# Kernel tuning notes

Measured on AMD Instinct MI355X. Metric: run time of the kernel, lower is better.

The kernel has to match this reference:

```python
import jax, jax.numpy as jnp
import numpy as np

N = 8192
IN_F = 512
OUT_F = 64
ALPHA = 0.2  # LeakyReLU negative slope
NEG_INF = -9e15


def setup_inputs() -> dict:
    key = jax.random.key(0)
    k1, k2, k3, k4 = jax.random.split(key, 4)
    # xavier_uniform-style scale (gain=1.414)
    w_bound = 1.414 * np.sqrt(6.0 / (IN_F + OUT_F))
    a_bound = 1.414 * np.sqrt(6.0 / (2 * OUT_F + 1))
    return {
        "input": jax.random.normal(k1, (N, IN_F), dtype=jnp.float32),
        "adj": jax.random.randint(k2, (N, N), 0, 2, dtype=jnp.int32),
        "W": jax.random.uniform(k3, (IN_F, OUT_F), jnp.float32, -w_bound, w_bound),
        "a": jax.random.uniform(k4, (2 * OUT_F, 1), jnp.float32, -a_bound, a_bound),
        "sig_sample_size": 512,
    }


def reference(input, adj, W, a, sig_sample_size):
    h = input @ W  # [N, F]
    # Split 'a' so e_ij = leakyrelu(a1.h_i + a2.h_j) without the N*N*2F repeat/cat
    a1, a2 = a[:OUT_F, 0], a[OUT_F:, 0]  # [F], [F]
    e = jax.nn.leaky_relu((h @ a1)[:, None] + (h @ a2)[None, :], negative_slope=ALPHA)  # [N, N]
    attention = jnp.where(adj > 0, e, NEG_INF)
    attention = jax.nn.softmax(attention, axis=1)
    sig_scores = jnp.sum(attention, axis=0)  # [N]
    _, indices = jax.lax.top_k(sig_scores, sig_sample_size)
    return indices
```

## Files before the change

kernel.cpp:

```cpp
#include <hip/hip_runtime.h>
#include <stdint.h>

#define NROW 8192
#define IN_F 512
#define OUT_F 64
#define ALPHA 0.2f

__device__ float  g_wa1[IN_F];
__device__ float  g_wa2[IN_F];
__device__ float  g_f1[NROW];
__device__ float  g_f2[NROW];
__device__ float  g_E2f[NROW];
__device__ float  g_F2f[NROW];
__device__ double g_E2d[NROW];
__device__ double g_F2d[NROW];
__device__ double g_accp[NROW];
__device__ double g_accn[NROW];
__device__ double g_G1[NROW];
__device__ double g_H1[NROW];
__device__ double g_colsum[NROW];
__device__ unsigned long long g_mask[(size_t)NROW * 128];

__global__ void prep_wa(const float* __restrict__ W, const float* __restrict__ a) {
    int k = threadIdx.x;
    if (k < IN_F) {
        double s1 = 0.0, s2 = 0.0;
        for (int t = 0; t < OUT_F; ++t) {
            double w = (double)W[k * OUT_F + t];
            s1 += w * (double)a[t];
            s2 += w * (double)a[OUT_F + t];
        }
        g_wa1[k] = (float)s1;
        g_wa2[k] = (float)s2;
        #pragma unroll
        for (int i = 0; i < 16; ++i) g_colsum[k * 16 + i] = 0.0;
    }
}

__global__ void __launch_bounds__(256) compute_f(const float* __restrict__ in) {
    int wave = threadIdx.x >> 6, lane = threadIdx.x & 63;
    int row = blockIdx.x * 4 + wave;
    const float4* in4  = (const float4*)(in + (size_t)row * IN_F);
    const float4* wa14 = (const float4*)g_wa1;
    const float4* wa24 = (const float4*)g_wa2;
    double s1 = 0.0, s2 = 0.0;
    #pragma unroll
    for (int half = 0; half < 2; ++half) {
        int idx = half * 64 + lane;
        float4 x = in4[idx];
        float4 u = wa14[idx];
        float4 v = wa24[idx];
        s1 += (double)x.x*u.x + (double)x.y*u.y + (double)x.z*u.z + (double)x.w*u.w;
        s2 += (double)x.x*v.x + (double)x.y*v.y + (double)x.z*v.z + (double)x.w*v.w;
    }
    #pragma unroll
    for (int off = 32; off > 0; off >>= 1) {
        s1 += __shfl_down(s1, off, 64);
        s2 += __shfl_down(s2, off, 64);
    }
    if (lane == 0) {
        float f1 = (float)s1, f2 = (float)s2;
        g_f1[row] = f1; g_f2[row] = f2;
        double e2 = exp((double)f2), g2 = exp(0.2 * (double)f2);
        g_E2d[row] = e2;        g_F2d[row] = g2;
        g_E2f[row] = (float)e2; g_F2f[row] = (float)g2;
    }
}

__global__ void __launch_bounds__(256) row_z_mask(const int* __restrict__ adj) {
    __shared__ float E2s[NROW];
    __shared__ float F2s[NROW];
    __shared__ double zp[16], zn[16];
    int tid = threadIdx.x;
    int wave = tid >> 6, lane = tid & 63;
    for (int k = tid; k < NROW / 4; k += 256) {
        ((float4*)E2s)[k] = ((const float4*)g_E2f)[k];
        ((float4*)F2s)[k] = ((const float4*)g_F2f)[k];
    }
    __syncthreads();
    int row0 = blockIdx.x * 4;
    for (int r = 0; r < 4; ++r) {
        int row = row0 + r;
        float f1r = g_f1[row];
        float Ft = expf(-0.2f * f1r);
        const int4* arow = (const int4*)(adj + (size_t)row * NROW) + wave * 512;
        unsigned long long myword = 0;
        double accp = 0.0, accn = 0.0;
        #pragma unroll
        for (int it = 0; it < 8; ++it) {
            int4 av = arow[it * 64 + lane];
            int colbase = wave * 2048 + it * 256 + lane * 4;
            float4 E2v = *(const float4*)&E2s[colbase];
            float4 F2v = *(const float4*)&F2s[colbase];
            bool p0 = av.x > 0, p1 = av.y > 0, p2 = av.z > 0, p3 = av.w > 0;
            unsigned long long b0 = __ballot(p0), b1 = __ballot(p1);
            unsigned long long b2 = __ballot(p2), b3 = __ballot(p3);
            int bl = it * 4;
            if (lane == bl)     myword = b0;
            if (lane == bl + 1) myword = b1;
            if (lane == bl + 2) myword = b2;
            if (lane == bl + 3) myword = b3;
            bool q0 = F2v.x > Ft, q1 = F2v.y > Ft, q2 = F2v.z > Ft, q3 = F2v.w > Ft;
            accp += (p0 && q0) ? (double)E2v.x : 0.0;
            accn += (p0 && !q0) ? (double)F2v.x : 0.0;
            accp += (p1 && q1) ? (double)E2v.y : 0.0;
            accn += (p1 && !q1) ? (double)F2v.y : 0.0;
            accp += (p2 && q2) ? (double)E2v.z : 0.0;
            accn += (p2 && !q2) ? (double)F2v.z : 0.0;
            accp += (p3 && q3) ? (double)E2v.w : 0.0;
            accn += (p3 && !q3) ? (double)F2v.w : 0.0;
        }
        if (lane < 32) g_mask[(size_t)row * 128 + wave * 32 + lane] = myword;
        #pragma unroll
        for (int off = 32; off > 0; off >>= 1) {
            accp += __shfl_down(accp, off, 64);
            accn += __shfl_down(accn, off, 64);
        }
        if (lane == 0) { zp[r * 4 + wave] = accp; zn[r * 4 + wave] = accn; }
    }
    __syncthreads();
    if (tid < 4) {
        g_accp[row0 + tid] = zp[tid*4+0] + zp[tid*4+1] + zp[tid*4+2] + zp[tid*4+3];
        g_accn[row0 + tid] = zn[tid*4+0] + zn[tid*4+1] + zn[tid*4+2] + zn[tid*4+3];
    }
}

__global__ void __launch_bounds__(256) prep_gh() {
    int i = blockIdx.x * 256 + threadIdx.x;
    double f1d = (double)g_f1[i];
    double e1 = exp(f1d), h1 = exp(0.2 * f1d);
    double Z = e1 * g_accp[i] + h1 * g_accn[i];
    double zinv = 1.0 / Z;
    g_G1[i] = e1 * zinv;
    g_H1[i] = h1 * zinv;
}

__global__ void __launch_bounds__(256) colsum_kernel() {
    __shared__ float  f1s[256];
    __shared__ double G1s[256], H1s[256];
    __shared__ unsigned long long msk[1024];
    int tid = threadIdx.x;
    int cb = blockIdx.x & 31;
    int rb = blockIdx.x >> 5;
    int j = cb * 256 + tid;
    float f2j = g_f2[j];
    int i0 = rb * 256;
    f1s[tid] = g_f1[i0 + tid];
    G1s[tid] = g_G1[i0 + tid];
    H1s[tid] = g_H1[i0 + tid];
    for (int t = tid; t < 1024; t += 256)
        msk[t] = g_mask[(size_t)(i0 + (t >> 2)) * 128 + cb * 4 + (t & 3)];
    __syncthreads();
    int c = tid & 3, bit = (tid >> 2) & 63;
    double accp = 0.0, accn = 0.0;
    for (int i = 0; i < 256; ++i) {
        unsigned long long wv = msk[i * 4 + c];
        bool b = (wv >> bit) & 1ULL;
        float e = f1s[i] + f2j;
        bool pos = e > 0.0f;
        accp += (b && pos)  ? G1s[i] : 0.0;
        accn += (b && !pos) ? H1s[i] : 0.0;
    }
    double res = g_E2d[j] * accp + g_F2d[j] * accn;
    atomicAdd(&g_colsum[j], res);
}

__global__ void __launch_bounds__(1024) topk_kernel(int* __restrict__ out, int K) {
    __shared__ unsigned int sbits[NROW];
    __shared__ unsigned int hist[256];
    __shared__ unsigned long long cand[1024];
    __shared__ unsigned long long s_prefix;
    __shared__ unsigned int s_want, s_cnt;
    int tid = threadIdx.x;
    for (int k = tid; k < NROW; k += 1024) {
        float s = (float)g_colsum[k];
        unsigned int u = __float_as_uint(s);
        u = (u & 0x80000000u) ? ~u : (u | 0x80000000u);
        sbits[k] = u;
    }
    if (tid == 0) { s_prefix = 0ULL; s_want = (unsigned)K; s_cnt = 0; }
    __syncthreads();
    for (int lvl = 0; lvl < 6; ++lvl) {
        int shift = 40 - lvl * 8;
        if (tid < 256) hist[tid] = 0;
        __syncthreads();
        unsigned long long pmask = (lvl == 0) ? 0ULL : (~0ULL << (shift + 8));
        unsigned long long prefix = s_prefix;
        for (int k = tid; k < NROW; k += 1024) {
            unsigned long long kk =
                ((unsigned long long)sbits[k] << 13) | (unsigned long long)(8191 - k);
            if ((kk & pmask) == prefix)
                atomicAdd(&hist[(unsigned)(kk >> shift) & 255u], 1u);
        }
        __syncthreads();
        if (tid == 0) {
            unsigned cum = 0; int b = 255;
            for (; b >= 0; --b) { cum += hist[b]; if (cum >= s_want) break; }
            if (b < 0) b = 0;
            s_want -= (cum - hist[b]);
            s_prefix |= ((unsigned long long)b << shift);
        }
        __syncthreads();
    }
    unsigned long long thr = s_prefix;
    for (int k = tid; k < NROW; k += 1024) {
        unsigned long long kk =
            ((unsigned long long)sbits[k] << 13) | (unsigned long long)(8191 - k);
        if (kk >= thr) {
            unsigned pos = atomicAdd(&s_cnt, 1u);
            if (pos < 1024u) cand[pos] = kk;
        }
    }
    __syncthreads();
    unsigned cnt = s_cnt;
    if ((unsigned)tid >= cnt) cand[tid] = 0ULL;
    __syncthreads();
    for (int k2 = 2; k2 <= 1024; k2 <<= 1) {
        for (int jj = k2 >> 1; jj > 0; jj >>= 1) {
            int ixj = tid ^ jj;
            if (ixj > tid) {
                unsigned long long a = cand[tid], b = cand[ixj];
                bool up = ((tid & k2) == 0);
                if (up ? (a < b) : (a > b)) { cand[tid] = b; cand[ixj] = a; }
            }
            __syncthreads();
        }
    }
    if (tid < K) out[tid] = 8191 - (int)(cand[tid] & 0x1FFFULL);
}

extern "C" void kernel_launch(void* const* d_in, const int* in_sizes, int n_in,
                              void* d_out, int out_size, void* d_ws, size_t ws_size,
                              hipStream_t stream) {
    const float* input = (const float*)d_in[0];
    const int*   adj   = (const int*)d_in[1];
    const float* W     = (const float*)d_in[2];
    const float* a     = (const float*)d_in[3];
    int* out = (int*)d_out;
    int K = out_size;

    prep_wa<<<1, 512, 0, stream>>>(W, a);
    compute_f<<<NROW / 4, 256, 0, stream>>>(input);
    row_z_mask<<<NROW / 4, 256, 0, stream>>>(adj);
    prep_gh<<<NROW / 256, 256, 0, stream>>>();
    colsum_kernel<<<1024, 256, 0, stream>>>();
    topk_kernel<<<1, 1024, 0, stream>>>(out, K);
}
```

Baseline: 513.4 us.

## Fuse normalizer into row pass, pack row data, use float accumulation, speed up top-k

Derives exp(f2) as the fifth power of exp(0.2 f2) so only one shared array is loaded per block. Folds the prep_gh kernel into row_z_mask's epilogue and packs f1, G1 and H1 into one float4 per row. colsum now accumulates in float instead of double. The top-k radix select skips levels whose byte is constant across all keys and uses wave-aggregated, per-wave histograms instead of contended atomics. These changes cut LDS traffic, one launch and the fp64 work, at the cost of slight precision loss that could reorder near-tied scores.

```diff
diff --git a/kernel.cpp b/kernel.cpp
--- a/kernel.cpp
+++ b/kernel.cpp
@@ -10,14 +10,10 @@
 __device__ float  g_wa2[IN_F];
 __device__ float  g_f1[NROW];
 __device__ float  g_f2[NROW];
-__device__ float  g_E2f[NROW];
 __device__ float  g_F2f[NROW];
 __device__ double g_E2d[NROW];
 __device__ double g_F2d[NROW];
-__device__ double g_accp[NROW];
-__device__ double g_accn[NROW];
-__device__ double g_G1[NROW];
-__device__ double g_H1[NROW];
+__device__ float4 g_pk[NROW];
 __device__ double g_colsum[NROW];
 __device__ unsigned long long g_mask[(size_t)NROW * 128];
 
@@ -62,21 +58,18 @@
         float f1 = (float)s1, f2 = (float)s2;
         g_f1[row] = f1; g_f2[row] = f2;
         double e2 = exp((double)f2), g2 = exp(0.2 * (double)f2);
-        g_E2d[row] = e2;        g_F2d[row] = g2;
-        g_E2f[row] = (float)e2; g_F2f[row] = (float)g2;
+        g_E2d[row] = e2; g_F2d[row] = g2;
+        g_F2f[row] = (float)g2;
     }
 }
 
 __global__ void __launch_bounds__(256) row_z_mask(const int* __restrict__ adj) {
-    __shared__ float E2s[NROW];
     __shared__ float F2s[NROW];
     __shared__ double zp[16], zn[16];
     int tid = threadIdx.x;
     int wave = tid >> 6, lane = tid & 63;
-    for (int k = tid; k < NROW / 4; k += 256) {
-        ((float4*)E2s)[k] = ((const float4*)g_E2f)[k];
+    for (int k = tid; k < NROW / 4; k += 256)
         ((float4*)F2s)[k] = ((const float4*)g_F2f)[k];
-    }
     __syncthreads();
     int row0 = blockIdx.x * 4;
     for (int r = 0; r < 4; ++r) {
@@ -90,7 +83,6 @@
         for (int it = 0; it < 8; ++it) {
             int4 av = arow[it * 64 + lane];
             int colbase = wave * 2048 + it * 256 + lane * 4;
-            float4 E2v = *(const float4*)&E2s[colbase];
             float4 F2v = *(const float4*)&F2s[colbase];
             bool p0 = av.x > 0, p1 = av.y > 0, p2 = av.z > 0, p3 = av.w > 0;
             unsigned long long b0 = __ballot(p0), b1 = __ballot(p1);
@@ -100,14 +92,19 @@
             if (lane == bl + 1) myword = b1;
             if (lane == bl + 2) myword = b2;
             if (lane == bl + 3) myword = b3;
+            float x2, e;
             bool q0 = F2v.x > Ft, q1 = F2v.y > Ft, q2 = F2v.z > Ft, q3 = F2v.w > Ft;
-            accp += (p0 && q0) ? (double)E2v.x : 0.0;
+            x2 = F2v.x * F2v.x; e = x2 * x2 * F2v.x;
+            accp += (p0 && q0)  ? (double)e     : 0.0;
             accn += (p0 && !q0) ? (double)F2v.x : 0.0;
-            accp += (p1 && q1) ? (double)E2v.y : 0.0;
+            x2 = F2v.y * F2v.y; e = x2 * x2 * F2v.y;
+            accp += (p1 && q1)  ? (double)e     : 0.0;
             accn += (p1 && !q1) ? (double)F2v.y : 0.0;
-            accp += (p2 && q2) ? (double)E2v.z : 0.0;
+            x2 = F2v.z * F2v.z; e = x2 * x2 * F2v.z;
+            accp += (p2 && q2)  ? (double)e     : 0.0;
             accn += (p2 && !q2) ? (double)F2v.z : 0.0;
-            accp += (p3 && q3) ? (double)E2v.w : 0.0;
+            x2 = F2v.w * F2v.w; e = x2 * x2 * F2v.w;
+            accp += (p3 && q3)  ? (double)e     : 0.0;
             accn += (p3 && !q3) ? (double)F2v.w : 0.0;
         }
         if (lane < 32) g_mask[(size_t)row * 128 + wave * 32 + lane] = myword;
@@ -120,24 +117,19 @@
     }
     __syncthreads();
     if (tid < 4) {
-        g_accp[row0 + tid] = zp[tid*4+0] + zp[tid*4+1] + zp[tid*4+2] + zp[tid*4+3];
-        g_accn[row0 + tid] = zn[tid*4+0] + zn[tid*4+1] + zn[tid*4+2] + zn[tid*4+3];
-    }
-}
-
-__global__ void __launch_bounds__(256) prep_gh() {
-    int i = blockIdx.x * 256 + threadIdx.x;
-    double f1d = (double)g_f1[i];
-    double e1 = exp(f1d), h1 = exp(0.2 * f1d);
-    double Z = e1 * g_accp[i] + h1 * g_accn[i];
-    double zinv = 1.0 / Z;
-    g_G1[i] = e1 * zinv;
-    g_H1[i] = h1 * zinv;
+        int row = row0 + tid;
+        double accp = zp[tid*4+0] + zp[tid*4+1] + zp[tid*4+2] + zp[tid*4+3];
+        double accn = zn[tid*4+0] + zn[tid*4+1] + zn[tid*4+2] + zn[tid*4+3];
+        float f1 = g_f1[row];
+        double f1d = (double)f1;
+        double e1 = exp(f1d), h1 = exp(0.2 * f1d);
+        double zinv = 1.0 / (e1 * accp + h1 * accn);
+        g_pk[row] = make_float4(f1, (float)(e1 * zinv), (float)(h1 * zinv), 0.0f);
+    }
 }
 
 __global__ void __launch_bounds__(256) colsum_kernel() {
-    __shared__ float  f1s[256];
-    __shared__ double G1s[256], H1s[256];
+    __shared__ float4 pks[256];
     __shared__ unsigned long long msk[1024];
     int tid = threadIdx.x;
     int cb = blockIdx.x & 31;
@@ -145,64 +137,102 @@
     int j = cb * 256 + tid;
     float f2j = g_f2[j];
     int i0 = rb * 256;
-    f1s[tid] = g_f1[i0 + tid];
-    G1s[tid] = g_G1[i0 + tid];
-    H1s[tid] = g_H1[i0 + tid];
+    pks[tid] = g_pk[i0 + tid];
     for (int t = tid; t < 1024; t += 256)
         msk[t] = g_mask[(size_t)(i0 + (t >> 2)) * 128 + cb * 4 + (t & 3)];
     __syncthreads();
     int c = tid & 3, bit = (tid >> 2) & 63;
-    double accp = 0.0, accn = 0.0;
+    float accp = 0.0f, accn = 0.0f;
     for (int i = 0; i < 256; ++i) {
         unsigned long long wv = msk[i * 4 + c];
+        float4 P = pks[i];
         bool b = (wv >> bit) & 1ULL;
-        float e = f1s[i] + f2j;
-        bool pos = e > 0.0f;
-        accp += (b && pos)  ? G1s[i] : 0.0;
-        accn += (b && !pos) ? H1s[i] : 0.0;
-    }
-    double res = g_E2d[j] * accp + g_F2d[j] * accn;
+        bool pos = (P.x + f2j) > 0.0f;
+        accp += (b && pos)  ? P.y : 0.0f;
+        accn += (b && !pos) ? P.z : 0.0f;
+    }
+    double res = g_E2d[j] * (double)accp + g_F2d[j] * (double)accn;
     atomicAdd(&g_colsum[j], res);
 }
 
 __global__ void __launch_bounds__(1024) topk_kernel(int* __restrict__ out, int K) {
     __shared__ unsigned int sbits[NROW];
-    __shared__ unsigned int hist[256];
+    __shared__ unsigned int shist[16 * 257];
+    __shared__ unsigned int ctot[256];
+    __shared__ unsigned long long wand[16], wor[16];
     __shared__ unsigned long long cand[1024];
-    __shared__ unsigned long long s_prefix;
-    __shared__ unsigned int s_want, s_cnt;
+    __shared__ unsigned int s_cnt;
     int tid = threadIdx.x;
+    int wave = tid >> 6, lane = tid & 63;
+
+    unsigned long long kand = ~0ULL, kor = 0ULL;
     for (int k = tid; k < NROW; k += 1024) {
         float s = (float)g_colsum[k];
         unsigned int u = __float_as_uint(s);
         u = (u & 0x80000000u) ? ~u : (u | 0x80000000u);
         sbits[k] = u;
-    }
-    if (tid == 0) { s_prefix = 0ULL; s_want = (unsigned)K; s_cnt = 0; }
-    __syncthreads();
+        unsigned long long kk =
+            ((unsigned long long)u << 13) | (unsigned long long)(8191 - k);
+        kand &= kk; kor |= kk;
+    }
+    #pragma unroll
+    for (int off = 32; off > 0; off >>= 1) {
+        kand &= __shfl_down(kand, off, 64);
+        kor  |= __shfl_down(kor,  off, 64);
+    }
+    if (lane == 0) { wand[wave] = kand; wor[wave] = kor; }
+    if (tid == 0) s_cnt = 0;
+    __syncthreads();
+    unsigned long long andR = ~0ULL, orR = 0ULL;
+    #pragma unroll
+    for (int w = 0; w < 16; ++w) { andR &= wand[w]; orR |= wor[w]; }
+    unsigned long long diff = andR ^ orR;
+
+    unsigned long long prefix = 0ULL;
+    unsigned int want = (unsigned)K;
     for (int lvl = 0; lvl < 6; ++lvl) {
         int shift = 40 - lvl * 8;
-        if (tid < 256) hist[tid] = 0;
+        unsigned int bdiff = (unsigned)(diff >> shift) & 255u;
+        if (bdiff == 0u) {
+            prefix |= ((andR >> shift) & 255ULL) << shift;
+            continue;
+        }
+        __syncthreads();
+        for (int t = tid; t < 16 * 257; t += 1024) shist[t] = 0;
         __syncthreads();
         unsigned long long pmask = (lvl == 0) ? 0ULL : (~0ULL << (shift + 8));
-        unsigned long long prefix = s_prefix;
         for (int k = tid; k < NROW; k += 1024) {
             unsigned long long kk =
                 ((unsigned long long)sbits[k] << 13) | (unsigned long long)(8191 - k);
-            if ((kk & pmask) == prefix)
-                atomicAdd(&hist[(unsigned)(kk >> shift) & 255u], 1u);
-        }
-        __syncthreads();
-        if (tid == 0) {
-            unsigned cum = 0; int b = 255;
-            for (; b >= 0; --b) { cum += hist[b]; if (cum >= s_want) break; }
-            if (b < 0) b = 0;
-            s_want -= (cum - hist[b]);
-            s_prefix |= ((unsigned long long)b << shift);
-        }
-        __syncthreads();
-    }
-    unsigned long long thr = s_prefix;
+            bool act = (kk & pmask) == (prefix & pmask);
+            unsigned int b = (unsigned)(kk >> shift) & 255u;
+            unsigned long long am = __ballot(act);
+            while (am) {
+                int src = __ffsll((long long)am) - 1;
+                unsigned int bb = (unsigned)__shfl((int)b, src, 64);
+                unsigned long long grp = __ballot(act && (b == bb));
+                if (lane == src)
+                    atomicAdd(&shist[wave * 257 + bb], (unsigned)__popcll(grp));
+                am &= ~grp;
+            }
+        }
+        __syncthreads();
+        if (tid < 256) {
+            unsigned int s = 0;
+            #pragma unroll
+            for (int w = 0; w < 16; ++w) s += shist[w * 257 + tid];
+            ctot[tid] = s;
+        }
+        __syncthreads();
+        unsigned int cum = 0; int b = 255;
+        for (; b >= 0; --b) { cum += ctot[b]; if (cum >= want) break; }
+        if (b < 0) b = 0;
+        want -= (cum - ctot[b]);
+        prefix |= ((unsigned long long)b << shift);
+    }
+
+    unsigned long long thr = prefix;
+    __syncthreads();
     for (int k = tid; k < NROW; k += 1024) {
         unsigned long long kk =
             ((unsigned long long)sbits[k] << 13) | (unsigned long long)(8191 - k);
@@ -219,9 +249,9 @@
         for (int jj = k2 >> 1; jj > 0; jj >>= 1) {
             int ixj = tid ^ jj;
             if (ixj > tid) {
-                unsigned long long a = cand[tid], b = cand[ixj];
+                unsigned long long a = cand[tid], bb = cand[ixj];
                 bool up = ((tid & k2) == 0);
-                if (up ? (a < b) : (a > b)) { cand[tid] = b; cand[ixj] = a; }
+                if (up ? (a < bb) : (a > bb)) { cand[tid] = bb; cand[ixj] = a; }
             }
             __syncthreads();
         }
@@ -242,7 +272,6 @@
     prep_wa<<<1, 512, 0, stream>>>(W, a);
     compute_f<<<NROW / 4, 256, 0, stream>>>(input);
     row_z_mask<<<NROW / 4, 256, 0, stream>>>(adj);
-    prep_gh<<<NROW / 256, 256, 0, stream>>>();
     colsum_kernel<<<1024, 256, 0, stream>>>();
     topk_kernel<<<1, 1024, 0, stream>>>(out, K);
 }
```

Result: no change. 513.7 us (+0.0%).
